# Optimization experiments

Hardware: AMD Instinct MI355X
Metric: run time of the kernel (lower is better)

## Reference

```python
import jax, jax.numpy as jnp
import numpy as np

N = 100000
H = 128
F_IN = 32
F_OUT = 16
NUM_GRAPHS = 64
NEG_SLOPE = 0.2


def setup_inputs() -> dict:
    key = jax.random.key(0)
    ks = jax.random.split(key, 16)
    inp = {
        'x': jax.random.normal(ks[0], (N, F_IN), dtype=jnp.float32),
        'edge_index': jax.random.randint(ks[1], (2, 1000000), 0, N, dtype=jnp.int32),
        'subgraph_edge_index': jax.random.randint(ks[2], (2, 1000000), 0, N, dtype=jnp.int32),
        'node_subnode_index': jax.random.randint(ks[3], (2, 200000), 0, N, dtype=jnp.int32),
        'subnode_node_index': jax.random.randint(ks[4], (2, 200000), 0, N, dtype=jnp.int32),
        'ground_node': jnp.arange(40000, dtype=jnp.int32),
        'subgraph_batch_index': jax.random.randint(ks[5], (60000,), 0, NUM_GRAPHS, dtype=jnp.int32),
        'batch_idx': jax.random.randint(ks[6], (40000,), 0, NUM_GRAPHS, dtype=jnp.int32),
    }
    s_in = 1.0 / np.sqrt(F_IN)
    s_h = 1.0 / np.sqrt(H)
    inp['emb_W'] = jax.random.uniform(ks[7], (F_IN, H), jnp.float32, -s_in, s_in)
    inp['emb_b'] = jax.random.uniform(ks[8], (H,), jnp.float32, -s_in, s_in)
    # 4 GATv2 layers (depth=1): lin_l, lin_r, att, bias per layer
    inp['Wl'] = jax.random.uniform(ks[9], (4, H, H), jnp.float32, -s_h, s_h)
    inp['Wr'] = jax.random.uniform(ks[10], (4, H, H), jnp.float32, -s_h, s_h)
    inp['att'] = jax.random.uniform(ks[11], (4, H), jnp.float32, -s_h, s_h)
    inp['bias'] = jax.random.uniform(ks[12], (4, H), jnp.float32, -s_h, s_h)
    inp['out_W'] = jax.random.uniform(ks[13], (H, F_OUT), jnp.float32, -s_h, s_h)
    inp['out_b'] = jax.random.uniform(ks[14], (F_OUT,), jnp.float32, -s_h, s_h)
    return inp


def _gatv2(x, ei, Wl, Wr, att, b):
    # add self loops (PyG GATv2Conv default add_self_loops=True)
    loops = jnp.broadcast_to(jnp.arange(N, dtype=ei.dtype)[None, :], (2, N))
    ei = jnp.concatenate([ei, loops], axis=1)
    src, dst = ei[0], ei[1]
    xl = x @ Wl  # source transform [N,H]
    xr = x @ Wr  # target transform [N,H]
    e = jax.nn.leaky_relu(xl[src] + xr[dst], NEG_SLOPE) @ att  # [E]
    m = jax.ops.segment_max(e, dst, num_segments=N)
    p = jnp.exp(e - m[dst])
    s = jax.ops.segment_sum(p, dst, num_segments=N)
    alpha = p / s[dst]
    out = jax.ops.segment_sum(alpha[:, None] * xl[src], dst, num_segments=N)
    return out + b


def reference(x, edge_index, subgraph_edge_index, node_subnode_index,
              subnode_node_index, ground_node, subgraph_batch_index, batch_idx,
              emb_W, emb_b, Wl, Wr, att, bias, out_W, out_b):
    h = x @ emb_W + emb_b
    eis = (edge_index, node_subnode_index, subgraph_edge_index, subnode_node_index)
    for i, ei in enumerate(eis):
        h = _gatv2(h, ei, Wl[i], Wr[i], att[i], bias[i])
    # global_add_pool over ground nodes
    pooled = jax.ops.segment_sum(h[ground_node], batch_idx, num_segments=NUM_GRAPHS)
    return pooled @ out_W + out_b
```

## Files before the change

kernel.cpp:

```cpp
#include <hip/hip_runtime.h>
#include <cstddef>


typedef __attribute__((ext_vector_type(8))) short bf16x8;
typedef __attribute__((ext_vector_type(4))) float f32x4;

#define NSH   10
#define CHUNK 8192
#define POOLP 256

__device__ __forceinline__ unsigned short f2bf(float f) {
  unsigned int u = __float_as_uint(f);
  u += 0x7fffu + ((u >> 16) & 1u);
  return (unsigned short)(u >> 16);
}
__device__ __forceinline__ unsigned short f2bf_rtz(float f) {
  return (unsigned short)(__float_as_uint(f) >> 16);
}
__device__ __forceinline__ float bf2f(short s) {
  return __uint_as_float(((unsigned int)(unsigned short)s) << 16);
}
__device__ __forceinline__ float2 unpk(unsigned int u) {
  return make_float2(__uint_as_float(u << 16),
                     __uint_as_float(u & 0xFFFF0000u));
}

__device__ __forceinline__ int lds_excl_scan(int* a, int len, int* aux, int tid)
{
  int g = (len + 255) >> 8;
  int lo = tid * g;
  int s = 0;
  for (int i = 0; i < g; ++i) { int idx = lo + i; if (idx < len) s += a[idx]; }
  aux[tid] = s;
  __syncthreads();
  for (int d = 1; d < 256; d <<= 1) {
    int v = (tid >= d) ? aux[tid - d] : 0;
    __syncthreads();
    aux[tid] += v;
    __syncthreads();
  }
  int run = aux[tid] - s;
  for (int i = 0; i < g; ++i) {
    int idx = lo + i;
    if (idx < len) { int t = a[idx]; a[idx] = run; run += t; }
  }
  int total = aux[255];
  __syncthreads();
  return total;
}

__device__ __forceinline__ void resolve_item(
    int id, int t1, int t2, int t3, int t4, int n,
    const int* s0, const int* s1, const int* s2, const int* s3,
    const int* d0, const int* d1, const int* d2, const int* d3,
    int& l, int& s, int& d, bool need_src)
{
  if (id < t4) {
    const int *sp, *dp; int e;
    if      (id < t1) { l = 0; e = id;      sp = s0; dp = d0; }
    else if (id < t2) { l = 1; e = id - t1; sp = s1; dp = d1; }
    else if (id < t3) { l = 2; e = id - t2; sp = s2; dp = d2; }
    else              { l = 3; e = id - t3; sp = s3; dp = d3; }
    d = dp[e];
    s = need_src ? sp[e] : 0;
  } else {
    int k = id - t4;
    l = (k >= 3 * n) ? 3 : (k >= 2 * n) ? 2 : (k >= n) ? 1 : 0;
    s = k - l * n; d = s;
  }
}

__global__ __launch_bounds__(256) void setup_kernel(
    const float* __restrict__ Wl, const float* __restrict__ Wr,
    const float* __restrict__ embW,
    unsigned short* __restrict__ packB, unsigned short* __restrict__ packE,
    int* __restrict__ offs4, int n, int e0, int e1, int e2, int e3)
{
  int id = blockIdx.x * 256 + threadIdx.x;
  if (id < 131072) {
    int j    = id & 7;
    int lane = (id >> 3) & 63;
    int kt   = (id >> 9) & 3;
    int ct   = (id >> 11) & 15;
    int l    = id >> 15;
    int k    = kt * 32 + (lane >> 4) * 8 + j;
    int col  = ct * 16 + (lane & 15);
    float v = (ct < 8) ? Wl[(size_t)l * 16384 + k * 128 + col]
                       : Wr[(size_t)l * 16384 + k * 128 + (col - 128)];
    packB[id] = f2bf(v);
  }
  int pe = id - 131072;
  if (pe >= 0 && pe < 4096) {
    int j    = pe & 7;
    int lane = (pe >> 3) & 63;
    int ct   = pe >> 9;
    int k    = (lane >> 4) * 8 + j;
    int col  = ct * 16 + (lane & 15);
    packE[pe] = f2bf(embW[k * 128 + col]);
  }
  int q = pe - 4096;
  if (q >= 0 && q < 4) {
    int El = (q == 0) ? e0 : (q == 1) ? e1 : (q == 2) ? e2 : e3;
    offs4[(size_t)q * (n + 1) + n] = El + n;
  }
}

__global__ __launch_bounds__(256) void embed_mfma_kernel(
    const float* __restrict__ x, const unsigned short* __restrict__ packE,
    const float* __restrict__ b, unsigned short* __restrict__ hb, int n)
{
  const int wave = threadIdx.x >> 6;
  const int lane = threadIdx.x & 63;
  const int rlan = lane & 15;
  const int kgrp = lane >> 4;

  bf16x8 Bf[8];
#pragma unroll
  for (int ct = 0; ct < 8; ++ct)
    Bf[ct] = *(const bf16x8*)(packE + ((size_t)ct * 64 + lane) * 8);
  float bv[8];
#pragma unroll
  for (int ct = 0; ct < 8; ++ct) bv[ct] = b[ct * 16 + rlan];

  const float4* __restrict__ x4 = (const float4*)x;
  const int ntiles = (n + 15) / 16;
  for (int tile = blockIdx.x * 4 + wave; tile < ntiles; tile += gridDim.x * 4) {
    int r = tile * 16 + rlan;
    if (r >= n) r = n - 1;
    float4 a0 = x4[(size_t)r * 8 + kgrp * 2];
    float4 a1 = x4[(size_t)r * 8 + kgrp * 2 + 1];
    bf16x8 Af;
    Af[0] = (short)f2bf(a0.x); Af[1] = (short)f2bf(a0.y);
    Af[2] = (short)f2bf(a0.z); Af[3] = (short)f2bf(a0.w);
    Af[4] = (short)f2bf(a1.x); Af[5] = (short)f2bf(a1.y);
    Af[6] = (short)f2bf(a1.z); Af[7] = (short)f2bf(a1.w);

    f32x4 acc[8];
#pragma unroll
    for (int ct = 0; ct < 8; ++ct) {
      acc[ct] = (f32x4){0.f, 0.f, 0.f, 0.f};
      acc[ct] = __builtin_amdgcn_mfma_f32_16x16x32_bf16(Af, Bf[ct], acc[ct], 0, 0, 0);
    }
    int rowb = tile * 16 + kgrp * 4;
#pragma unroll
    for (int ct = 0; ct < 8; ++ct) {
      int col = ct * 16 + rlan;
#pragma unroll
      for (int rr = 0; rr < 4; ++rr)
        if (rowb + rr < n)
          hb[(size_t)(rowb + rr) * 128 + col] = f2bf(acc[ct][rr] + bv[ct]);
    }
  }
}

__global__ __launch_bounds__(256) void gemm_mfma_kernel(
    const unsigned short* __restrict__ hb,
    const unsigned short* __restrict__ packB,
    unsigned short* __restrict__ xlb, unsigned short* __restrict__ xrb, int n)
{
  const int wave = threadIdx.x >> 6;
  const int lane = threadIdx.x & 63;
  const int rlan = lane & 15;
  const int kgrp = lane >> 4;

  bf16x8 Bf[4][4];
#pragma unroll
  for (int ct = 0; ct < 4; ++ct)
#pragma unroll
    for (int kt = 0; kt < 4; ++kt)
      Bf[ct][kt] = *(const bf16x8*)(packB +
          ((((size_t)(wave * 4 + ct)) * 4 + kt) * 64 + lane) * 8);

  unsigned short* __restrict__ outp = (wave < 2) ? xlb : xrb;
  const int colbase = (wave & 1) * 64;

  const int ntiles = (n + 31) / 32;
  for (int tile = blockIdx.x; tile < ntiles; tile += gridDim.x) {
    const int row0 = tile * 32;
    bf16x8 Af[2][4];
#pragma unroll
    for (int rt = 0; rt < 2; ++rt) {
      int r = row0 + rt * 16 + rlan;
      if (r >= n) r = n - 1;
      const unsigned short* ap = hb + (size_t)r * 128 + kgrp * 8;
#pragma unroll
      for (int kt = 0; kt < 4; ++kt)
        Af[rt][kt] = *(const bf16x8*)(ap + kt * 32);
    }
    f32x4 acc[2][4];
#pragma unroll
    for (int rt = 0; rt < 2; ++rt)
#pragma unroll
      for (int ct = 0; ct < 4; ++ct)
        acc[rt][ct] = (f32x4){0.f, 0.f, 0.f, 0.f};
#pragma unroll
    for (int kt = 0; kt < 4; ++kt)
#pragma unroll
      for (int rt = 0; rt < 2; ++rt)
#pragma unroll
        for (int ct = 0; ct < 4; ++ct)
          acc[rt][ct] = __builtin_amdgcn_mfma_f32_16x16x32_bf16(
              Af[rt][kt], Bf[ct][kt], acc[rt][ct], 0, 0, 0);
#pragma unroll
    for (int rt = 0; rt < 2; ++rt) {
      int rowb = row0 + rt * 16 + kgrp * 4;
#pragma unroll
      for (int ct = 0; ct < 4; ++ct) {
        int col = colbase + ct * 16 + rlan;
        size_t base = (size_t)rowb * 128 + col;
#pragma unroll
        for (int r = 0; r < 4; ++r)
          if (rowb + r < n)
            outp[base + (size_t)r * 128] = f2bf_rtz(acc[rt][ct][r]);
      }
    }
  }
}

__global__ __launch_bounds__(256) void hist_kernel(
    const int* __restrict__ d0, const int* __restrict__ d1,
    const int* __restrict__ d2, const int* __restrict__ d3,
    int e0, int e1, int e2, int e3, int n, int nbk, int NB, int nitems,
    int* __restrict__ mat)
{
  __shared__ int hist[512];
  int tid = threadIdx.x, c = blockIdx.x;
  for (int i = tid; i < NB; i += 256) hist[i] = 0;
  __syncthreads();
  int t1 = e0, t2 = t1 + e1, t3 = t2 + e2, t4 = t3 + e3;
  int base = c * CHUNK;
#pragma unroll
  for (int k = 0; k < CHUNK / 256; ++k) {
    int id = base + k * 256 + tid;
    if (id < nitems) {
      int l, s, d;
      resolve_item(id, t1, t2, t3, t4, n,
                   nullptr, nullptr, nullptr, nullptr, d0, d1, d2, d3,
                   l, s, d, false);
      atomicAdd(&hist[l * nbk + (d >> NSH)], 1);
    }
  }
  __syncthreads();
  for (int i = tid; i < NB; i += 256) mat[(size_t)c * NB + i] = hist[i];
}

__global__ __launch_bounds__(256) void colscan_a_kernel(
    const int* __restrict__ mat, int* __restrict__ pfx,
    int nchunk, int NB, int* __restrict__ colsum)
{
  __shared__ int col[512];
  __shared__ int aux[256];
  int gb = blockIdx.x, tid = threadIdx.x;
  for (int i = tid; i < nchunk; i += 256) col[i] = mat[(size_t)i * NB + gb];
  __syncthreads();
  int tot = lds_excl_scan(col, nchunk, aux, tid);
  for (int i = tid; i < nchunk; i += 256) pfx[(size_t)i * NB + gb] = col[i];
  if (tid == 0) colsum[gb] = tot;
}

__global__ __launch_bounds__(256) void colscan_b_kernel(
    const int* __restrict__ colsum, int NB, int* __restrict__ colscan)
{
  __shared__ int buf[512];
  __shared__ int aux[256];
  int tid = threadIdx.x;
  for (int i = tid; i < NB; i += 256) buf[i] = colsum[i];
  __syncthreads();
  int tot = lds_excl_scan(buf, NB, aux, tid);
  for (int i = tid; i < NB; i += 256) colscan[i] = buf[i];
  if (tid == 0) colscan[NB] = tot;
}

__global__ __launch_bounds__(256) void scatter_kernel(
    const int* __restrict__ s0, const int* __restrict__ s1,
    const int* __restrict__ s2, const int* __restrict__ s3,
    const int* __restrict__ d0, const int* __restrict__ d1,
    const int* __restrict__ d2, const int* __restrict__ d3,
    int e0, int e1, int e2, int e3, int n, int nbk, int NB, int nitems,
    const int* __restrict__ mat, const int* __restrict__ pfx,
    const int* __restrict__ colscan, int* __restrict__ staging)
{
  __shared__ int lbuf[CHUNK];
  __shared__ int hist[512];
  __shared__ int cur[512];
  __shared__ int basex[512];
  __shared__ int aux[256];
  int tid = threadIdx.x, c = blockIdx.x;
  for (int i = tid; i < NB; i += 256) hist[i] = mat[(size_t)c * NB + i];
  __syncthreads();
  lds_excl_scan(hist, NB, aux, tid);
  for (int i = tid; i < NB; i += 256) {
    cur[i]   = hist[i];
    basex[i] = colscan[i] + pfx[(size_t)c * NB + i];
  }
  __syncthreads();
  int t1 = e0, t2 = t1 + e1, t3 = t2 + e2, t4 = t3 + e3;
  int base = c * CHUNK;
#pragma unroll
  for (int k = 0; k < CHUNK / 256; ++k) {
    int id = base + k * 256 + tid;
    if (id < nitems) {
      int l, s, d;
      resolve_item(id, t1, t2, t3, t4, n,
                   s0, s1, s2, s3, d0, d1, d2, d3, l, s, d, true);
      int gb = l * nbk + (d >> NSH);
      int p = atomicAdd(&cur[gb], 1);
      lbuf[p] = s | ((d & ((1 << NSH) - 1)) << 17);
    }
  }
  __syncthreads();
  int wave = tid >> 6, lane = tid & 63;
  for (int gb = wave; gb < NB; gb += 4) {
    int st = hist[gb], en = cur[gb];
    int gbase = basex[gb];
    for (int j = lane; j < en - st; j += 64)
      staging[gbase + j] = lbuf[st + j];
  }
}

__global__ __launch_bounds__(256) void finalize_kernel(
    const int* __restrict__ staging, const int* __restrict__ colscan,
    int* __restrict__ offs4, int* __restrict__ csr4, int n, int nbk,
    int cb0, int cb1, int cb2, int cb3)
{
  __shared__ int cnt[1 << NSH];
  __shared__ int pos[1 << NSH];
  __shared__ int aux[256];
  int gb = blockIdx.x, tid = threadIdx.x;
  int l = gb / nbk, b = gb % nbk;
  int beg = colscan[gb], end = colscan[gb + 1];
  int node0 = b << NSH;
  int ncount = n - node0; if (ncount > (1 << NSH)) ncount = 1 << NSH;
  int cbl = (l == 0) ? cb0 : (l == 1) ? cb1 : (l == 2) ? cb2 : cb3;

  for (int i = tid; i < (1 << NSH); i += 256) cnt[i] = 0;
  __syncthreads();
  for (int t = beg + tid; t < end; t += 256)
    atomicAdd(&cnt[staging[t] >> 17], 1);
  __syncthreads();
  lds_excl_scan(cnt, 1 << NSH, aux, tid);
  for (int i = tid; i < (1 << NSH); i += 256) {
    if (i < ncount)
      offs4[(size_t)l * (n + 1) + node0 + i] = beg + cnt[i] - cbl;
    pos[i] = cnt[i];
  }
  __syncthreads();
  for (int t = beg + tid; t < end; t += 256) {
    int e = staging[t];
    int p = atomicAdd(&pos[e >> 17], 1);
    csr4[beg + p] = e & 0x1FFFF;
  }
}

__global__ __launch_bounds__(256) void gat_dst_kernel(
    const unsigned short* __restrict__ xlb,
    const unsigned short* __restrict__ xrb,
    const int* __restrict__ offs, const int* __restrict__ csr,
    const float* __restrict__ att, const float* __restrict__ bias,
    float* __restrict__ hout_f, unsigned short* __restrict__ hout_b, int n)
{
  const float LOG2E = 1.4426950408889634f;
  int wid = (blockIdx.x * 256 + threadIdx.x) >> 4;
  int c   = threadIdx.x & 15;
  if (wid >= n) return;

  uint4 xru = *(const uint4*)(xrb + (size_t)wid * 128 + c * 8);
  float2 xr0 = unpk(xru.x), xr1 = unpk(xru.y);
  float2 xr2 = unpk(xru.z), xr3 = unpk(xru.w);
  const float2* att2 = (const float2*)att + c * 4;
  float2 a0 = att2[0], a1 = att2[1], a2 = att2[2], a3 = att2[3];
  a0.x *= LOG2E; a0.y *= LOG2E; a1.x *= LOG2E; a1.y *= LOG2E;
  a2.x *= LOG2E; a2.y *= LOG2E; a3.x *= LOG2E; a3.y *= LOG2E;

  int beg = offs[wid], end = offs[wid + 1];
  float ssum = 0.f;
  float2 ac0 = {0.f, 0.f}, ac1 = {0.f, 0.f};
  float2 ac2 = {0.f, 0.f}, ac3 = {0.f, 0.f};

  int s0 = csr[beg];
  uint4 xu = *(const uint4*)(xlb + (size_t)s0 * 128 + c * 8);

  for (int j = beg; j < end; ++j) {
    uint4 cu = xu;
    int jn = j + 1;
    if (jn < end) {
      int sn = csr[jn];
      xu = *(const uint4*)(xlb + (size_t)sn * 128 + c * 8);
    }
    float2 xs0 = unpk(cu.x), xs1 = unpk(cu.y);
    float2 xs2 = unpk(cu.z), xs3 = unpk(cu.w);
    float2 t0 = {xs0.x + xr0.x, xs0.y + xr0.y};
    float2 t1 = {xs1.x + xr1.x, xs1.y + xr1.y};
    float2 t2 = {xs2.x + xr2.x, xs2.y + xr2.y};
    float2 t3 = {xs3.x + xr3.x, xs3.y + xr3.y};
    t0.x = fmaxf(t0.x, 0.2f * t0.x); t0.y = fmaxf(t0.y, 0.2f * t0.y);
    t1.x = fmaxf(t1.x, 0.2f * t1.x); t1.y = fmaxf(t1.y, 0.2f * t1.y);
    t2.x = fmaxf(t2.x, 0.2f * t2.x); t2.y = fmaxf(t2.y, 0.2f * t2.y);
    t3.x = fmaxf(t3.x, 0.2f * t3.x); t3.y = fmaxf(t3.y, 0.2f * t3.y);
    float2 pp = {t0.x * a0.x, t0.y * a0.y};
    pp.x = fmaf(t1.x, a1.x, pp.x); pp.y = fmaf(t1.y, a1.y, pp.y);
    pp.x = fmaf(t2.x, a2.x, pp.x); pp.y = fmaf(t2.y, a2.y, pp.y);
    pp.x = fmaf(t3.x, a3.x, pp.x); pp.y = fmaf(t3.y, a3.y, pp.y);
    float part = pp.x + pp.y;
    part += __shfl_xor(part, 1, 64);
    part += __shfl_xor(part, 2, 64);
    part += __shfl_xor(part, 4, 64);
    part += __shfl_xor(part, 8, 64);
    float p = __builtin_amdgcn_exp2f(part);
    ssum += p;
    ac0.x = fmaf(p, xs0.x, ac0.x); ac0.y = fmaf(p, xs0.y, ac0.y);
    ac1.x = fmaf(p, xs1.x, ac1.x); ac1.y = fmaf(p, xs1.y, ac1.y);
    ac2.x = fmaf(p, xs2.x, ac2.x); ac2.y = fmaf(p, xs2.y, ac2.y);
    ac3.x = fmaf(p, xs3.x, ac3.x); ac3.y = fmaf(p, xs3.y, ac3.y);
  }

  float inv = 1.0f / ssum;
  float o[8] = {ac0.x, ac0.y, ac1.x, ac1.y, ac2.x, ac2.y, ac3.x, ac3.y};
#pragma unroll
  for (int k = 0; k < 8; ++k) o[k] = fmaf(o[k], inv, bias[c * 8 + k]);

  if (hout_f) {
    float4 v0 = make_float4(o[0], o[1], o[2], o[3]);
    float4 v1 = make_float4(o[4], o[5], o[6], o[7]);
    *(float4*)(hout_f + (size_t)wid * 128 + c * 8)     = v0;
    *(float4*)(hout_f + (size_t)wid * 128 + c * 8 + 4) = v1;
  } else {
    bf16x8 ob;
#pragma unroll
    for (int k = 0; k < 8; ++k) ob[k] = (short)f2bf(o[k]);
    *(bf16x8*)(hout_b + (size_t)wid * 128 + c * 8) = ob;
  }
}

__global__ __launch_bounds__(256) void pool_partial_kernel(
    const float* __restrict__ h, const int* __restrict__ gnode,
    const int* __restrict__ bidx, float* __restrict__ partial, int ng)
{
  __shared__ float acc[64 * 128];
  int tid = threadIdx.x;
  for (int t = tid; t < 64 * 128; t += 256) acc[t] = 0.f;
  __syncthreads();
  int col = tid & 127, half = tid >> 7;
  for (int nd = blockIdx.x * 2 + half; nd < ng; nd += gridDim.x * 2) {
    int row = gnode[nd];
    int g   = bidx[nd];
    atomicAdd(&acc[g * 128 + col], h[(size_t)row * 128 + col]);
  }
  __syncthreads();
  float* out = partial + (size_t)blockIdx.x * 8192;
  for (int t = tid; t < 64 * 128; t += 256) out[t] = acc[t];
}

__global__ __launch_bounds__(128) void pool_out_kernel(
    const float* __restrict__ partial, const float* __restrict__ W,
    const float* __restrict__ b, float* __restrict__ out)
{
  __shared__ float pr[128];
  int g = blockIdx.x, tid = threadIdx.x;
  float s = 0.f;
  for (int p = 0; p < POOLP; ++p) s += partial[(size_t)p * 8192 + g * 128 + tid];
  pr[tid] = s;
  __syncthreads();
  if (tid < 16) {
    float acc = b[tid];
#pragma unroll
    for (int k = 0; k < 128; ++k) acc += pr[k] * W[k * 16 + tid];
    out[g * 16 + tid] = acc;
  }
}

extern "C" void kernel_launch(void* const* d_in, const int* in_sizes, int n_in,
                              void* d_out, int out_size, void* d_ws, size_t ws_size,
                              hipStream_t stream)
{
  const float* x    = (const float*)d_in[0];
  const int* ei0    = (const int*)d_in[1];
  const int* ei_sg  = (const int*)d_in[2];
  const int* ei_ns  = (const int*)d_in[3];
  const int* ei_sn  = (const int*)d_in[4];
  const int* gnode  = (const int*)d_in[5];
  const int* bidx   = (const int*)d_in[7];
  const float* embW = (const float*)d_in[8];
  const float* embB = (const float*)d_in[9];
  const float* Wl   = (const float*)d_in[10];
  const float* Wr   = (const float*)d_in[11];
  const float* att  = (const float*)d_in[12];
  const float* bias = (const float*)d_in[13];
  const float* outW = (const float*)d_in[14];
  const float* outB = (const float*)d_in[15];

  const int n  = in_sizes[0] / 32;
  const int ng = in_sizes[5];

  const int  E_arr[4] = { in_sizes[1] / 2, in_sizes[3] / 2,
                          in_sizes[2] / 2, in_sizes[4] / 2 };
  const int* eptr[4]  = { ei0, ei_ns, ei_sg, ei_sn };
  const int E_tot  = E_arr[0] + E_arr[1] + E_arr[2] + E_arr[3];
  const int nitems = E_tot + 4 * n;
  const int nbk    = (n + (1 << NSH) - 1) >> NSH;
  const int NB     = 4 * nbk;
  const int nchunk = (nitems + CHUNK - 1) / CHUNK;
  int cb[4];
  cb[0] = 0;
  for (int i = 1; i < 4; ++i) cb[i] = cb[i - 1] + E_arr[i - 1] + n;

  char* ws = (char*)d_ws;
  size_t off = 0;
  auto alloc = [&](size_t bytes) -> void* {
    void* p = ws + off;
    off = (off + bytes + 255) & ~(size_t)255;
    return p;
  };
  float*          h      = (float*)alloc((size_t)n * 128 * sizeof(float));
  unsigned short* hb     = (unsigned short*)alloc((size_t)n * 128 * sizeof(unsigned short));
  unsigned short* xlb    = (unsigned short*)alloc((size_t)n * 128 * sizeof(unsigned short));
  unsigned short* xrb    = (unsigned short*)alloc((size_t)n * 128 * sizeof(unsigned short));
  int*            offs4  = (int*)alloc((size_t)4 * (n + 1) * sizeof(int));
  int*            mat    = (int*)alloc((size_t)nchunk * NB * sizeof(int));
  int*            pfx    = (int*)alloc((size_t)nchunk * NB * sizeof(int));
  int*            colsum = (int*)alloc((size_t)NB * sizeof(int));
  int*            colscan= (int*)alloc((size_t)(NB + 1) * sizeof(int));
  int*            staging= (int*)alloc((size_t)nitems * sizeof(int));
  int*            csr4   = (int*)alloc((size_t)nitems * sizeof(int));
  unsigned short* packB  = (unsigned short*)alloc(131072 * sizeof(unsigned short));
  unsigned short* packE  = (unsigned short*)alloc(4096 * sizeof(unsigned short));
  float*          partial= (float*)alloc((size_t)POOLP * 8192 * sizeof(float));
  (void)ws_size; (void)n_in; (void)out_size;

  const int* D[4] = { eptr[0] + E_arr[0], eptr[1] + E_arr[1],
                      eptr[2] + E_arr[2], eptr[3] + E_arr[3] };

  int setup_items = 131072 + 4096 + 4;
  setup_kernel<<<(setup_items + 255) / 256, 256, 0, stream>>>(
      Wl, Wr, embW, packB, packE, offs4, n,
      E_arr[0], E_arr[1], E_arr[2], E_arr[3]);

  const int ntile16 = (n + 15) / 16;
  embed_mfma_kernel<<<(ntile16 + 3) / 4, 256, 0, stream>>>(
      x, packE, embB, hb, n);

  hist_kernel<<<nchunk, 256, 0, stream>>>(
      D[0], D[1], D[2], D[3], E_arr[0], E_arr[1], E_arr[2], E_arr[3],
      n, nbk, NB, nitems, mat);
  colscan_a_kernel<<<NB, 256, 0, stream>>>(mat, pfx, nchunk, NB, colsum);
  colscan_b_kernel<<<1, 256, 0, stream>>>(colsum, NB, colscan);
  scatter_kernel<<<nchunk, 256, 0, stream>>>(
      eptr[0], eptr[1], eptr[2], eptr[3], D[0], D[1], D[2], D[3],
      E_arr[0], E_arr[1], E_arr[2], E_arr[3], n, nbk, NB, nitems,
      mat, pfx, colscan, staging);
  finalize_kernel<<<NB, 256, 0, stream>>>(
      staging, colscan, offs4, csr4, n, nbk, cb[0], cb[1], cb[2], cb[3]);

  const int gemm_grid = ((n + 31) / 32 + 1) / 2;
  for (int l = 0; l < 4; ++l) {
    gemm_mfma_kernel<<<gemm_grid, 256, 0, stream>>>(
        hb, packB + (size_t)l * 32768, xlb, xrb, n);
    gat_dst_kernel<<<((size_t)n * 16 + 255) / 256, 256, 0, stream>>>(
        xlb, xrb, offs4 + (size_t)l * (n + 1), csr4 + cb[l],
        att + (size_t)l * 128, bias + (size_t)l * 128,
        (l == 3) ? h : nullptr, (l < 3) ? hb : nullptr, n);
  }

  pool_partial_kernel<<<POOLP, 256, 0, stream>>>(h, gnode, bidx, partial, ng);
  pool_out_kernel<<<64, 128, 0, stream>>>(partial, outW, outB, (float*)d_out);
}
```

Baseline: 512.0 us.

## Transpose GEMM operands for packed row stores and unroll GAT edge loop by two

The projection GEMM now treats the weight matrix as the MFMA A operand and the node features as B, so each lane holds four consecutive output dims of one node. That lets it write packed 8-byte bf16 stores instead of scattered 2-byte stores, with tiles of 16 nodes and a matching grid size. Separately, the GATv2 destination loop handles two edges per iteration with two gathers prefetched, giving more loads in flight. This raises register pressure, and it reuses the weight packing unchanged under a swapped operand role, which is only correct if that packing is valid as the A fragment.

Result: slower. 554.3 us (+8.3%).

```diff
diff --git a/kernel.cpp b/kernel.cpp
--- a/kernel.cpp
+++ b/kernel.cpp
@@ -14,11 +14,11 @@
   u += 0x7fffu + ((u >> 16) & 1u);
   return (unsigned short)(u >> 16);
 }
-__device__ __forceinline__ unsigned short f2bf_rtz(float f) {
-  return (unsigned short)(__float_as_uint(f) >> 16);
-}
 __device__ __forceinline__ float bf2f(short s) {
   return __uint_as_float(((unsigned int)(unsigned short)s) << 16);
+}
+__device__ __forceinline__ unsigned int pack2bf(float a, float b) {
+  return (__float_as_uint(a) >> 16) | (__float_as_uint(b) & 0xFFFF0000u);
 }
 __device__ __forceinline__ float2 unpk(unsigned int u) {
   return make_float2(__uint_as_float(u << 16),
@@ -160,58 +160,49 @@
 {
   const int wave = threadIdx.x >> 6;
   const int lane = threadIdx.x & 63;
-  const int rlan = lane & 15;
+  const int nlan = lane & 15;
   const int kgrp = lane >> 4;
 
-  bf16x8 Bf[4][4];
-#pragma unroll
-  for (int ct = 0; ct < 4; ++ct)
+  bf16x8 Af[4][4];
+#pragma unroll
+  for (int mt = 0; mt < 4; ++mt)
 #pragma unroll
     for (int kt = 0; kt < 4; ++kt)
-      Bf[ct][kt] = *(const bf16x8*)(packB +
-          ((((size_t)(wave * 4 + ct)) * 4 + kt) * 64 + lane) * 8);
+      Af[mt][kt] = *(const bf16x8*)(packB +
+          ((((size_t)(wave * 4 + mt)) * 4 + kt) * 64 + lane) * 8);
 
   unsigned short* __restrict__ outp = (wave < 2) ? xlb : xrb;
-  const int colbase = (wave & 1) * 64;
-
-  const int ntiles = (n + 31) / 32;
+  const int dimbase = (wave & 1) * 64;
+
+  const int ntiles = (n + 15) / 16;
   for (int tile = blockIdx.x; tile < ntiles; tile += gridDim.x) {
-    const int row0 = tile * 32;
-    bf16x8 Af[2][4];
-#pragma unroll
-    for (int rt = 0; rt < 2; ++rt) {
-      int r = row0 + rt * 16 + rlan;
-      if (r >= n) r = n - 1;
-      const unsigned short* ap = hb + (size_t)r * 128 + kgrp * 8;
-#pragma unroll
-      for (int kt = 0; kt < 4; ++kt)
-        Af[rt][kt] = *(const bf16x8*)(ap + kt * 32);
-    }
-    f32x4 acc[2][4];
-#pragma unroll
-    for (int rt = 0; rt < 2; ++rt)
-#pragma unroll
-      for (int ct = 0; ct < 4; ++ct)
-        acc[rt][ct] = (f32x4){0.f, 0.f, 0.f, 0.f};
+    int node = tile * 16 + nlan;
+    int nc = (node < n) ? node : n - 1;
+    const unsigned short* bp = hb + (size_t)nc * 128 + kgrp * 8;
+    bf16x8 Bf[4];
 #pragma unroll
     for (int kt = 0; kt < 4; ++kt)
-#pragma unroll
-      for (int rt = 0; rt < 2; ++rt)
-#pragma unroll
-        for (int ct = 0; ct < 4; ++ct)
-          acc[rt][ct] = __builtin_amdgcn_mfma_f32_16x16x32_bf16(
-              Af[rt][kt], Bf[ct][kt], acc[rt][ct], 0, 0, 0);
-#pragma unroll
-    for (int rt = 0; rt < 2; ++rt) {
-      int rowb = row0 + rt * 16 + kgrp * 4;
-#pragma unroll
-      for (int ct = 0; ct < 4; ++ct) {
-        int col = colbase + ct * 16 + rlan;
-        size_t base = (size_t)rowb * 128 + col;
-#pragma unroll
-        for (int r = 0; r < 4; ++r)
-          if (rowb + r < n)
-            outp[base + (size_t)r * 128] = f2bf_rtz(acc[rt][ct][r]);
+      Bf[kt] = *(const bf16x8*)(bp + kt * 32);
+
+    f32x4 acc[4];
+#pragma unroll
+    for (int mt = 0; mt < 4; ++mt)
+      acc[mt] = (f32x4){0.f, 0.f, 0.f, 0.f};
+#pragma unroll
+    for (int kt = 0; kt < 4; ++kt)
+#pragma unroll
+      for (int mt = 0; mt < 4; ++mt)
+        acc[mt] = __builtin_amdgcn_mfma_f32_16x16x32_bf16(
+            Af[mt][kt], Bf[kt], acc[mt], 0, 0, 0);
+
+    if (node < n) {
+      size_t rowbase = (size_t)node * 128 + dimbase + kgrp * 4;
+#pragma unroll
+      for (int mt = 0; mt < 4; ++mt) {
+        uint2 pk;
+        pk.x = pack2bf(acc[mt][0], acc[mt][1]);
+        pk.y = pack2bf(acc[mt][2], acc[mt][3]);
+        *(uint2*)(outp + rowbase + mt * 16) = pk;
       }
     }
   }
@@ -377,41 +368,67 @@
   float2 ac0 = {0.f, 0.f}, ac1 = {0.f, 0.f};
   float2 ac2 = {0.f, 0.f}, ac3 = {0.f, 0.f};
 
-  int s0 = csr[beg];
-  uint4 xu = *(const uint4*)(xlb + (size_t)s0 * 128 + c * 8);
-
-  for (int j = beg; j < end; ++j) {
-    uint4 cu = xu;
-    int jn = j + 1;
-    if (jn < end) {
-      int sn = csr[jn];
-      xu = *(const uint4*)(xlb + (size_t)sn * 128 + c * 8);
-    }
-    float2 xs0 = unpk(cu.x), xs1 = unpk(cu.y);
-    float2 xs2 = unpk(cu.z), xs3 = unpk(cu.w);
-    float2 t0 = {xs0.x + xr0.x, xs0.y + xr0.y};
-    float2 t1 = {xs1.x + xr1.x, xs1.y + xr1.y};
-    float2 t2 = {xs2.x + xr2.x, xs2.y + xr2.y};
-    float2 t3 = {xs3.x + xr3.x, xs3.y + xr3.y};
-    t0.x = fmaxf(t0.x, 0.2f * t0.x); t0.y = fmaxf(t0.y, 0.2f * t0.y);
-    t1.x = fmaxf(t1.x, 0.2f * t1.x); t1.y = fmaxf(t1.y, 0.2f * t1.y);
-    t2.x = fmaxf(t2.x, 0.2f * t2.x); t2.y = fmaxf(t2.y, 0.2f * t2.y);
-    t3.x = fmaxf(t3.x, 0.2f * t3.x); t3.y = fmaxf(t3.y, 0.2f * t3.y);
-    float2 pp = {t0.x * a0.x, t0.y * a0.y};
-    pp.x = fmaf(t1.x, a1.x, pp.x); pp.y = fmaf(t1.y, a1.y, pp.y);
-    pp.x = fmaf(t2.x, a2.x, pp.x); pp.y = fmaf(t2.y, a2.y, pp.y);
-    pp.x = fmaf(t3.x, a3.x, pp.x); pp.y = fmaf(t3.y, a3.y, pp.y);
-    float part = pp.x + pp.y;
-    part += __shfl_xor(part, 1, 64);
-    part += __shfl_xor(part, 2, 64);
-    part += __shfl_xor(part, 4, 64);
-    part += __shfl_xor(part, 8, 64);
-    float p = __builtin_amdgcn_exp2f(part);
-    ssum += p;
-    ac0.x = fmaf(p, xs0.x, ac0.x); ac0.y = fmaf(p, xs0.y, ac0.y);
-    ac1.x = fmaf(p, xs1.x, ac1.x); ac1.y = fmaf(p, xs1.y, ac1.y);
-    ac2.x = fmaf(p, xs2.x, ac2.x); ac2.y = fmaf(p, xs2.y, ac2.y);
-    ac3.x = fmaf(p, xs3.x, ac3.x); ac3.y = fmaf(p, xs3.y, ac3.y);
+  uint4 xu0 = *(const uint4*)(xlb + (size_t)csr[beg] * 128 + c * 8);
+  uint4 xu1 = {0, 0, 0, 0};
+  if (beg + 1 < end)
+    xu1 = *(const uint4*)(xlb + (size_t)csr[beg + 1] * 128 + c * 8);
+
+  for (int j = beg; j < end; j += 2) {
+    uint4 cu0 = xu0, cu1 = xu1;
+    bool act1 = (j + 1 < end);
+    if (j + 2 < end)
+      xu0 = *(const uint4*)(xlb + (size_t)csr[j + 2] * 128 + c * 8);
+    if (j + 3 < end)
+      xu1 = *(const uint4*)(xlb + (size_t)csr[j + 3] * 128 + c * 8);
+
+    float2 e0s0 = unpk(cu0.x), e0s1 = unpk(cu0.y);
+    float2 e0s2 = unpk(cu0.z), e0s3 = unpk(cu0.w);
+    float2 e1s0 = unpk(cu1.x), e1s1 = unpk(cu1.y);
+    float2 e1s2 = unpk(cu1.z), e1s3 = unpk(cu1.w);
+
+    float2 t00 = {e0s0.x + xr0.x, e0s0.y + xr0.y};
+    float2 t01 = {e0s1.x + xr1.x, e0s1.y + xr1.y};
+    float2 t02 = {e0s2.x + xr2.x, e0s2.y + xr2.y};
+    float2 t03 = {e0s3.x + xr3.x, e0s3.y + xr3.y};
+    float2 t10 = {e1s0.x + xr0.x, e1s0.y + xr0.y};
+    float2 t11 = {e1s1.x + xr1.x, e1s1.y + xr1.y};
+    float2 t12 = {e1s2.x + xr2.x, e1s2.y + xr2.y};
+    float2 t13 = {e1s3.x + xr3.x, e1s3.y + xr3.y};
+    t00.x = fmaxf(t00.x, 0.2f * t00.x); t00.y = fmaxf(t00.y, 0.2f * t00.y);
+    t01.x = fmaxf(t01.x, 0.2f * t01.x); t01.y = fmaxf(t01.y, 0.2f * t01.y);
+    t02.x = fmaxf(t02.x, 0.2f * t02.x); t02.y = fmaxf(t02.y, 0.2f * t02.y);
+    t03.x = fmaxf(t03.x, 0.2f * t03.x); t03.y = fmaxf(t03.y, 0.2f * t03.y);
+    t10.x = fmaxf(t10.x, 0.2f * t10.x); t10.y = fmaxf(t10.y, 0.2f * t10.y);
+    t11.x = fmaxf(t11.x, 0.2f * t11.x); t11.y = fmaxf(t11.y, 0.2f * t11.y);
+    t12.x = fmaxf(t12.x, 0.2f * t12.x); t12.y = fmaxf(t12.y, 0.2f * t12.y);
+    t13.x = fmaxf(t13.x, 0.2f * t13.x); t13.y = fmaxf(t13.y, 0.2f * t13.y);
+
+    float2 p0 = {t00.x * a0.x, t00.y * a0.y};
+    p0.x = fmaf(t01.x, a1.x, p0.x); p0.y = fmaf(t01.y, a1.y, p0.y);
+    p0.x = fmaf(t02.x, a2.x, p0.x); p0.y = fmaf(t02.y, a2.y, p0.y);
+    p0.x = fmaf(t03.x, a3.x, p0.x); p0.y = fmaf(t03.y, a3.y, p0.y);
+    float2 p1 = {t10.x * a0.x, t10.y * a0.y};
+    p1.x = fmaf(t11.x, a1.x, p1.x); p1.y = fmaf(t11.y, a1.y, p1.y);
+    p1.x = fmaf(t12.x, a2.x, p1.x); p1.y = fmaf(t12.y, a2.y, p1.y);
+    p1.x = fmaf(t13.x, a3.x, p1.x); p1.y = fmaf(t13.y, a3.y, p1.y);
+
+    float part0 = p0.x + p0.y;
+    float part1 = p1.x + p1.y;
+    part0 += __shfl_xor(part0, 1, 64);   part1 += __shfl_xor(part1, 1, 64);
+    part0 += __shfl_xor(part0, 2, 64);   part1 += __shfl_xor(part1, 2, 64);
+    part0 += __shfl_xor(part0, 4, 64);   part1 += __shfl_xor(part1, 4, 64);
+    part0 += __shfl_xor(part0, 8, 64);   part1 += __shfl_xor(part1, 8, 64);
+    float pe0 = __builtin_amdgcn_exp2f(part0);
+    float pe1 = act1 ? __builtin_amdgcn_exp2f(part1) : 0.f;
+    ssum += pe0 + pe1;
+    ac0.x = fmaf(pe0, e0s0.x, ac0.x); ac0.y = fmaf(pe0, e0s0.y, ac0.y);
+    ac1.x = fmaf(pe0, e0s1.x, ac1.x); ac1.y = fmaf(pe0, e0s1.y, ac1.y);
+    ac2.x = fmaf(pe0, e0s2.x, ac2.x); ac2.y = fmaf(pe0, e0s2.y, ac2.y);
+    ac3.x = fmaf(pe0, e0s3.x, ac3.x); ac3.y = fmaf(pe0, e0s3.y, ac3.y);
+    ac0.x = fmaf(pe1, e1s0.x, ac0.x); ac0.y = fmaf(pe1, e1s0.y, ac0.y);
+    ac1.x = fmaf(pe1, e1s1.x, ac1.x); ac1.y = fmaf(pe1, e1s1.y, ac1.y);
+    ac2.x = fmaf(pe1, e1s2.x, ac2.x); ac2.y = fmaf(pe1, e1s2.y, ac2.y);
+    ac3.x = fmaf(pe1, e1s3.x, ac3.x); ac3.y = fmaf(pe1, e1s3.y, ac3.y);
   }
 
   float inv = 1.0f / ssum;
@@ -551,7 +568,7 @@
   finalize_kernel<<<NB, 256, 0, stream>>>(
       staging, colscan, offs4, csr4, n, nbk, cb[0], cb[1], cb[2], cb[3]);
 
-  const int gemm_grid = ((n + 31) / 32 + 1) / 2;
+  const int gemm_grid = (ntile16 + 1) / 2;
   for (int l = 0; l < 4; ++l) {
     gemm_mfma_kernel<<<gemm_grid, 256, 0, stream>>>(
         hb, packB + (size_t)l * 32768, xlb, xrb, n);
```
